# Kernel tuning notes

Measured on AMD Instinct MI355X. Metric: run time of the kernel, lower is better.

Reference implementation:

```python
import jax, jax.numpy as jnp
import numpy as np

N = 50000      # nodes
E = 1600000    # edges
IN = 128       # in_feats
H = 4          # heads
F = 32         # per-head feats (h_feats = out_feats = 32)
NEG_SLOPE = 0.2


def setup_inputs() -> dict:
    key = jax.random.key(0)
    ks = jax.random.split(key, 12)
    glorot = lambda k, shape: jax.random.normal(k, shape, jnp.float32) * np.sqrt(2.0 / (shape[0] + shape[-1])).astype(np.float32)
    x = jax.random.normal(ks[0], (N, IN), jnp.float32)
    edge_index = jax.random.randint(ks[1], (2, E), 0, N, dtype=jnp.int32)
    W1 = glorot(ks[2], (IN, H * F))
    att_src1 = glorot(ks[3], (H, F))
    att_dst1 = glorot(ks[4], (H, F))
    b1 = jnp.zeros((F,), jnp.float32)
    W2 = glorot(ks[5], (F, H * F))
    att_src2 = glorot(ks[6], (H, F))
    att_dst2 = glorot(ks[7], (H, F))
    b2 = jnp.zeros((F,), jnp.float32)
    return {"x": x, "edge_index": edge_index,
            "W1": W1, "att_src1": att_src1, "att_dst1": att_dst1, "b1": b1,
            "W2": W2, "att_src2": att_src2, "att_dst2": att_dst2, "b2": b2}


def gat_conv(x, edge_index, W, a_src, a_dst, bias):
    """PyG GATConv with concat=False (head-average), add_self_loops=True."""
    n = x.shape[0]
    h = (x @ W).reshape(n, H, F)                      # [N,H,F]
    loops = jnp.arange(n, dtype=edge_index.dtype)
    src = jnp.concatenate([edge_index[0], loops])     # [E+N]
    dst = jnp.concatenate([edge_index[1], loops])
    alpha_src = jnp.einsum('nhf,hf->nh', h, a_src)    # [N,H]
    alpha_dst = jnp.einsum('nhf,hf->nh', h, a_dst)
    e = jax.nn.leaky_relu(alpha_src[src] + alpha_dst[dst], NEG_SLOPE)  # [E+N,H]
    # scatter-softmax over incoming edges per destination node
    m = jax.ops.segment_max(e, dst, num_segments=n)
    e = jnp.exp(e - m[dst])
    s = jax.ops.segment_sum(e, dst, num_segments=n)
    alpha = e / (s[dst] + 1e-16)                      # [E+N,H]
    out = jax.ops.segment_sum(alpha[:, :, None] * h[src], dst, num_segments=n)  # [N,H,F]
    return out.mean(axis=1) + bias                    # concat=False: average heads


def reference(x, edge_index, W1, att_src1, att_dst1, b1, W2, att_src2, att_dst2, b2):
    h = gat_conv(x, edge_index, W1, att_src1, att_dst1, b1)
    h = jax.nn.elu(h)
    return gat_conv(h, edge_index, W2, att_src2, att_dst2, b2)
```

## Files before the change

kernel.cpp:

```cpp
#include <hip/hip_runtime.h>
#include <hip/hip_bf16.h>
#include <hip/hip_fp16.h>
#include <math.h>


#define NS 64
#define NB_S 4
#define MAXNPB_S 12500
#define NB_H 8
#define MAXNPB_H 6272

typedef unsigned int u32x4 __attribute__((ext_vector_type(4)));

__device__ __forceinline__ float lrelu(float x) { return x > 0.f ? x : 0.2f * x; }

__device__ __forceinline__ unsigned int fenc(float f) {
    unsigned int u = __float_as_uint(f);
    return (u & 0x80000000u) ? ~u : (u | 0x80000000u);
}
__device__ __forceinline__ float fdec(unsigned int e) {
    unsigned int u = (e & 0x80000000u) ? (e & 0x7FFFFFFFu) : ~e;
    return __uint_as_float(u);
}

__device__ __forceinline__ unsigned short f2bf(float x) {
    unsigned u = __float_as_uint(x);
    return (unsigned short)((u + 0x7FFFu + ((u >> 16) & 1u)) >> 16);
}
__device__ __forceinline__ float bflo(unsigned w) { return __uint_as_float(w << 16); }
__device__ __forceinline__ float bfhi(unsigned w) { return __uint_as_float(w & 0xFFFF0000u); }

__device__ __forceinline__ unsigned pack_h2(float a, float b) {
    const __half2 h = __float22half2_rn(make_float2(a, b));
    return *(const unsigned*)&h;
}
__device__ __forceinline__ float2 unpack_h2(unsigned w) {
    __half2 h = *(const __half2*)&w;
    return __half22float2(h);
}

__global__ __launch_bounds__(256) void scan_part(unsigned short* __restrict__ cnt_priv,
                                                 int* __restrict__ deg,
                                                 int* __restrict__ bsum, int n) {
    __shared__ int red[256];
    const int t = threadIdx.x;
    const int node = blockIdx.x * 256 + t;
    int run = 0;
    if (node < n) {
#pragma unroll 4
        for (int s = 0; s < NS; ++s) {
            unsigned short* p = &cnt_priv[(size_t)s * n + node];
            const int c = *p;
            *p = (unsigned short)run;
            run += c;
        }
        deg[node] = run;
    }
    red[t] = (node < n) ? run : 0;
    __syncthreads();
    for (int o = 128; o > 0; o >>= 1) {
        if (t < o) red[t] += red[t + o];
        __syncthreads();
    }
    if (t == 0) bsum[blockIdx.x] = red[0];
}

__global__ __launch_bounds__(256) void scan_mid(const int* __restrict__ bsum,
                                                int* __restrict__ boff, int nb,
                                                int* __restrict__ rowptr, int n) {
    __shared__ int s[256];
    const int t = threadIdx.x;
    const int v = (t < nb) ? bsum[t] : 0;
    s[t] = v;
    __syncthreads();
    for (int o = 1; o < 256; o <<= 1) {
        const int u = (t >= o) ? s[t - o] : 0;
        __syncthreads();
        s[t] += u;
        __syncthreads();
    }
    if (t < nb) boff[t] = s[t] - v;
    if (t == 255) rowptr[n] = s[255];
}

__global__ __launch_bounds__(256) void scan_final(const int* __restrict__ deg,
                                                  const int* __restrict__ boff,
                                                  int* __restrict__ rowptr, int n) {
    __shared__ int s[256];
    const int t = threadIdx.x;
    const int i = blockIdx.x * 256 + t;
    const int v = (i < n) ? deg[i] : 0;
    s[t] = v;
    __syncthreads();
    for (int o = 1; o < 256; o <<= 1) {
        const int u = (t >= o) ? s[t - o] : 0;
        __syncthreads();
        s[t] += u;
        __syncthreads();
    }
    if (i < n) rowptr[i] = boff[blockIdx.x] + s[t] - v;
}

__global__ __launch_bounds__(512) void scatter_kernel(
    const int* __restrict__ src, const int* __restrict__ dst,
    const int* __restrict__ rowptr, const unsigned short* __restrict__ cnt_priv,
    const float* __restrict__ asrc, const float* __restrict__ adst,
    const unsigned int* __restrict__ gmax,
    uint4* __restrict__ esd, int E, int n, int npb) {
    __shared__ int cur[MAXNPB_S];
    const int b = blockIdx.x & (NB_S - 1);
    const int s = blockIdx.x / NB_S;
    const int lo = b * npb;
    const int hi = min(lo + npb, n);
    const int span = hi - lo;
    if (span <= 0) return;
    {
        const unsigned short* cp = cnt_priv + (size_t)s * n + lo;
        const int* rp = rowptr + lo;
        for (int j = threadIdx.x; j < span; j += 512) cur[j] = rp[j] + (int)cp[j];
    }
    __syncthreads();
    const char* aB = (const char*)asrc;
    const char* dB = (const char*)adst;
    const float g0 = fdec(gmax[0]), g1 = fdec(gmax[1]);
    const float g2 = fdec(gmax[2]), g3 = fdec(gmax[3]);

    auto place = [&](int sv, int dv) {
        const int p = atomicAdd(&cur[dv - lo], 1);
        const unsigned s16 = (unsigned)(sv << 4);
        const unsigned d16 = (unsigned)(dv << 4);
        const float4 as = *(const float4*)(aB + s16);
        const float4 ad = *(const float4*)(dB + d16);
        const float q0 = __expf(lrelu(as.x + ad.x) - lrelu(g0 + ad.x));
        const float q1 = __expf(lrelu(as.y + ad.y) - lrelu(g1 + ad.y));
        const float q2 = __expf(lrelu(as.z + ad.z) - lrelu(g2 + ad.z));
        const float q3 = __expf(lrelu(as.w + ad.w) - lrelu(g3 + ad.w));
        esd[p] = make_uint4(s16, d16, pack_h2(q0, q1), pack_h2(q2, q3));
    };

    const int E4 = E >> 2;
    const int len4 = (E4 + NS - 1) / NS;
    const int beg4 = s * len4;
    const int end4 = min(beg4 + len4, E4);
    const int4* dst4 = (const int4*)dst;
    const int4* src4 = (const int4*)src;
    for (int i = beg4 + threadIdx.x; i < end4; i += 512) {
        const int4 d = dst4[i];
        const int4 sv = src4[i];
        if (d.x >= lo && d.x < hi) place(sv.x, d.x);
        if (d.y >= lo && d.y < hi) place(sv.y, d.y);
        if (d.z >= lo && d.z < hi) place(sv.z, d.z);
        if (d.w >= lo && d.w < hi) place(sv.w, d.w);
    }
    if (s == NS - 1) {
        for (int i = (E4 << 2) + threadIdx.x; i < E; i += 512) {
            const int d = dst[i];
            if (d >= lo && d < hi) place(src[i], d);
        }
    }
}

__global__ __launch_bounds__(256) void edge_w_kernel(
    uint4* __restrict__ esd,
    const float* __restrict__ asrc, const float* __restrict__ adst,
    const unsigned int* __restrict__ gmax, int Etot) {
    const char* aB = (const char*)asrc;
    const char* dB = (const char*)adst;
    const float g0 = fdec(gmax[0]), g1 = fdec(gmax[1]);
    const float g2 = fdec(gmax[2]), g3 = fdec(gmax[3]);
    for (int i = blockIdx.x * blockDim.x + threadIdx.x; i < Etot;
         i += gridDim.x * blockDim.x) {
        const unsigned long long sd =
            __builtin_nontemporal_load((const unsigned long long*)&esd[i]);
        const unsigned s16 = (unsigned)sd;
        const unsigned d16 = (unsigned)(sd >> 32);
        const float4 as = *(const float4*)(aB + s16);
        const float4 ad = *(const float4*)(dB + d16);
        const float q0 = __expf(lrelu(as.x + ad.x) - lrelu(g0 + ad.x));
        const float q1 = __expf(lrelu(as.y + ad.y) - lrelu(g1 + ad.y));
        const float q2 = __expf(lrelu(as.z + ad.z) - lrelu(g2 + ad.z));
        const float q3 = __expf(lrelu(as.w + ad.w) - lrelu(g3 + ad.w));
        const unsigned long long rec =
            ((unsigned long long)pack_h2(q2, q3) << 32) | pack_h2(q0, q1);
        __builtin_nontemporal_store(
            rec, (unsigned long long*)((char*)&esd[i] + 8));
    }
}

template <int K>
__global__ __launch_bounds__(256) void gemm_hist(
    const float* __restrict__ X, const float* __restrict__ W,
    const float* __restrict__ AttS, const float* __restrict__ AttD,
    unsigned short* __restrict__ Hb, float* __restrict__ asrc, float* __restrict__ adst,
    unsigned int* __restrict__ gmax, int n, int gemmGrid,
    const int* __restrict__ dst, unsigned short* __restrict__ cnt_priv,
    int E, int npbH) {
    constexpr int GEMM_BYTES = 64 * K * 4;
    constexpr int HIST_BYTES = (K == 128) ? (MAXNPB_H * 4) : 0;
    constexpr int SMEM_BYTES = (GEMM_BYTES > HIST_BYTES) ? GEMM_BYTES : HIST_BYTES;
    __shared__ __align__(16) char smem[SMEM_BYTES];
    __shared__ unsigned int smax[4];
    const int tid = threadIdx.x;

    if constexpr (K == 128) {
        if (blockIdx.x >= gemmGrid) {
            int* h = (int*)smem;
            const int hb = blockIdx.x - gemmGrid;
            const int b = hb & (NB_H - 1);
            const int s = hb / NB_H;
            const int lo = b * npbH;
            const int hi = min(lo + npbH, n);
            const int span = hi - lo;
            if (span <= 0) return;
            for (int j = tid; j < span; j += 256) h[j] = 0;
            __syncthreads();
            const int E4 = E >> 2;
            const int len4 = (E4 + NS - 1) / NS;
            const int beg4 = s * len4;
            const int end4 = min(beg4 + len4, E4);
            const int4* dst4 = (const int4*)dst;
            for (int i = beg4 + tid; i < end4; i += 256) {
                const int4 d = dst4[i];
                if (d.x >= lo && d.x < hi) atomicAdd(&h[d.x - lo], 1);
                if (d.y >= lo && d.y < hi) atomicAdd(&h[d.y - lo], 1);
                if (d.z >= lo && d.z < hi) atomicAdd(&h[d.z - lo], 1);
                if (d.w >= lo && d.w < hi) atomicAdd(&h[d.w - lo], 1);
            }
            if (s == NS - 1) {
                for (int i = (E4 << 2) + tid; i < E; i += 256) {
                    const int d = dst[i];
                    if (d >= lo && d < hi) atomicAdd(&h[d - lo], 1);
                }
            }
            __syncthreads();
            unsigned short* outp = cnt_priv + (size_t)s * n + lo;
            for (int j = tid; j < span; j += 256) outp[j] = (unsigned short)h[j];
            return;
        }
    }

    float* Xs = (float*)smem;
    const int r = tid >> 5;
    const int sub = tid & 31;
    const int head = sub >> 3;
    const int pos = ((head & 1) << 1) | (head >> 1);
    const int fc = (sub & 7) * 4;
    const int rowBase = blockIdx.x * 64;

    if (tid < 4) smax[tid] = 0u;
    {
        const float4* X4 = (const float4*)X;
        float4* Xs4 = (float4*)Xs;
        const int K4 = K / 4;
        for (int i = tid; i < 64 * K4; i += 256) {
            int rr = rowBase + i / K4;
            Xs4[i] = (rr < n) ? X4[(size_t)rr * K4 + (i % K4)] : make_float4(0.f, 0.f, 0.f, 0.f);
        }
    }
    __syncthreads();

    float acc[8][4] = {};
    const float4* W4g = (const float4*)W;
#pragma unroll 4
    for (int k = 0; k < K; k += 4) {
        float4 wv[4];
#pragma unroll
        for (int j = 0; j < 4; ++j) wv[j] = W4g[(k + j) * 32 + sub];
        float4 xv[8];
#pragma unroll
        for (int b = 0; b < 8; ++b)
            xv[b] = *(const float4*)&Xs[(b * 8 + r) * K + k];
#pragma unroll
        for (int b = 0; b < 8; ++b) {
            acc[b][0] = fmaf(xv[b].x, wv[0].x, acc[b][0]);
            acc[b][1] = fmaf(xv[b].x, wv[0].y, acc[b][1]);
            acc[b][2] = fmaf(xv[b].x, wv[0].z, acc[b][2]);
            acc[b][3] = fmaf(xv[b].x, wv[0].w, acc[b][3]);
            acc[b][0] = fmaf(xv[b].y, wv[1].x, acc[b][0]);
            acc[b][1] = fmaf(xv[b].y, wv[1].y, acc[b][1]);
            acc[b][2] = fmaf(xv[b].y, wv[1].z, acc[b][2]);
            acc[b][3] = fmaf(xv[b].y, wv[1].w, acc[b][3]);
            acc[b][0] = fmaf(xv[b].z, wv[2].x, acc[b][0]);
            acc[b][1] = fmaf(xv[b].z, wv[2].y, acc[b][1]);
            acc[b][2] = fmaf(xv[b].z, wv[2].z, acc[b][2]);
            acc[b][3] = fmaf(xv[b].z, wv[2].w, acc[b][3]);
            acc[b][0] = fmaf(xv[b].w, wv[3].x, acc[b][0]);
            acc[b][1] = fmaf(xv[b].w, wv[3].y, acc[b][1]);
            acc[b][2] = fmaf(xv[b].w, wv[3].z, acc[b][2]);
            acc[b][3] = fmaf(xv[b].w, wv[3].w, acc[b][3]);
        }
    }

    float a_s[4], a_d[4];
#pragma unroll
    for (int j = 0; j < 4; ++j) {
        a_s[j] = AttS[head * 32 + fc + j];
        a_d[j] = AttD[head * 32 + fc + j];
    }
#pragma unroll
    for (int b = 0; b < 8; ++b) {
        const int row = rowBase + b * 8 + r;
        const float p0 = __shfl_xor(acc[b][0], 16);
        const float p1 = __shfl_xor(acc[b][1], 16);
        const float p2 = __shfl_xor(acc[b][2], 16);
        const float p3 = __shfl_xor(acc[b][3], 16);
        if (row < n) {
            if (head < 2) {
                char* base = (char*)Hb + (size_t)row * 256 + (unsigned)fc * 8 + head * 4;
                *(unsigned*)(base + 0)  = (unsigned)f2bf(acc[b][0]) | ((unsigned)f2bf(p0) << 16);
                *(unsigned*)(base + 8)  = (unsigned)f2bf(acc[b][1]) | ((unsigned)f2bf(p1) << 16);
                *(unsigned*)(base + 16) = (unsigned)f2bf(acc[b][2]) | ((unsigned)f2bf(p2) << 16);
                *(unsigned*)(base + 24) = (unsigned)f2bf(acc[b][3]) | ((unsigned)f2bf(p3) << 16);
            }
            float ps = acc[b][0] * a_s[0] + acc[b][1] * a_s[1] +
                       acc[b][2] * a_s[2] + acc[b][3] * a_s[3];
            float pd = acc[b][0] * a_d[0] + acc[b][1] * a_d[1] +
                       acc[b][2] * a_d[2] + acc[b][3] * a_d[3];
#pragma unroll
            for (int msk = 1; msk < 8; msk <<= 1) {
                ps += __shfl_xor(ps, msk);
                pd += __shfl_xor(pd, msk);
            }
            if ((sub & 7) == 0) {
                asrc[row * 4 + pos] = ps;
                adst[row * 4 + pos] = pd;
                atomicMax(&smax[pos], fenc(ps));
            }
        }
    }
    __syncthreads();
    if (tid < 4) atomicMax(&gmax[tid], smax[tid]);
}

__global__ __launch_bounds__(256) void node_kernel(
    const int* __restrict__ rowptr, const uint4* __restrict__ esd,
    const unsigned short* __restrict__ Hb, const float* __restrict__ asrc,
    const float* __restrict__ adst, const unsigned int* __restrict__ gmax,
    const float* __restrict__ bias,
    float* __restrict__ outp, int n, int apply_elu) {
    const int node = blockIdx.x * 8 + (threadIdx.x >> 5);
    if (node >= n) return;
    const unsigned f = threadIdx.x & 31;
    const unsigned f8 = f * 8;
    const char* hB = (const char*)Hb;
    const u32x4* eB = (const u32x4*)esd;

    const int beg = rowptr[node], end = rowptr[node + 1];
    const float4 ad4 = *(const float4*)(adst + (size_t)node * 4);
    const float4 as4 = *(const float4*)(asrc + (size_t)node * 4);
    const float M0 = lrelu(fdec(gmax[0]) + ad4.x);
    const float M1 = lrelu(fdec(gmax[1]) + ad4.y);
    const float M2 = lrelu(fdec(gmax[2]) + ad4.z);
    const float M3 = lrelu(fdec(gmax[3]) + ad4.w);

    const float q0 = __expf(lrelu(as4.x + ad4.x) - M0);
    const float q1 = __expf(lrelu(as4.y + ad4.y) - M1);
    const float q2 = __expf(lrelu(as4.z + ad4.z) - M2);
    const float q3 = __expf(lrelu(as4.w + ad4.w) - M3);
    float s0 = q0, s1 = q1, s2 = q2, s3 = q3;
    const uint2 hs = *(const uint2*)(hB + ((size_t)node << 8) + f8);
    float a0 = q0 * bflo(hs.x);
    float a1 = q1 * bfhi(hs.x);
    float a2 = q2 * bflo(hs.y);
    float a3 = q3 * bfhi(hs.y);

    int i = beg;
    for (; i + 8 <= end; i += 8) {
        u32x4 e[8];
#pragma unroll
        for (int u = 0; u < 8; ++u)
            e[u] = __builtin_nontemporal_load(&eB[i + u]);
        uint2 h[8];
#pragma unroll
        for (int u = 0; u < 8; ++u)
            h[u] = *(const uint2*)(hB + (((unsigned)e[u].x) << 4) + f8);
#pragma unroll
        for (int u = 0; u < 8; ++u) {
            const float2 qa = unpack_h2(e[u].z);
            const float2 qb = unpack_h2(e[u].w);
            s0 += qa.x; s1 += qa.y; s2 += qb.x; s3 += qb.y;
            a0 = fmaf(qa.x, bflo(h[u].x), a0);
            a1 = fmaf(qa.y, bfhi(h[u].x), a1);
            a2 = fmaf(qb.x, bflo(h[u].y), a2);
            a3 = fmaf(qb.y, bfhi(h[u].y), a3);
        }
    }
    for (; i < end; ++i) {
        const u32x4 e = __builtin_nontemporal_load(&eB[i]);
        const uint2 h = *(const uint2*)(hB + (((unsigned)e.x) << 4) + f8);
        const float2 qa = unpack_h2(e.z);
        const float2 qb = unpack_h2(e.w);
        s0 += qa.x; s1 += qa.y; s2 += qb.x; s3 += qb.y;
        a0 = fmaf(qa.x, bflo(h.x), a0);
        a1 = fmaf(qa.y, bfhi(h.x), a1);
        a2 = fmaf(qb.x, bflo(h.y), a2);
        a3 = fmaf(qb.y, bfhi(h.y), a3);
    }

    float v = a0 / s0 + a1 / s1 + a2 / s2 + a3 / s3;
    v = v * 0.25f + bias[f];
    if (apply_elu) v = (v > 0.f) ? v : (__expf(v) - 1.f);
    outp[(size_t)node * 32 + f] = v;
}


extern "C" void kernel_launch(void* const* d_in, const int* in_sizes, int n_in,
                              void* d_out, int out_size, void* d_ws, size_t ws_size,
                              hipStream_t stream) {
    const int N = in_sizes[0] / 128;
    const int E = in_sizes[1] / 2;
    const float* x = (const float*)d_in[0];
    const int* ei = (const int*)d_in[1];
    const float* W1 = (const float*)d_in[2];
    const float* atS1 = (const float*)d_in[3];
    const float* atD1 = (const float*)d_in[4];
    const float* b1 = (const float*)d_in[5];
    const float* W2 = (const float*)d_in[6];
    const float* atS2 = (const float*)d_in[7];
    const float* atD2 = (const float*)d_in[8];
    const float* b2 = (const float*)d_in[9];
    float* out = (float*)d_out;

    char* ws = (char*)d_ws;
    size_t off = 0;
    auto alloc = [&](size_t bytes) {
        void* p = ws + off;
        off = (off + bytes + 255) & ~(size_t)255;
        return p;
    };
    unsigned int* gmax = (unsigned int*)alloc(8 * sizeof(unsigned int));
    unsigned short* cnt_priv = (unsigned short*)alloc((size_t)NS * N * 2);
    int* deg = (int*)alloc((size_t)N * 4);
    int* rowptr = (int*)alloc((size_t)(N + 1) * 4);
    int* bsum = (int*)alloc(256 * 4);
    int* boff = (int*)alloc(256 * 4);
    uint4* esd = (uint4*)alloc((size_t)E * 16);
    unsigned short* hb = (unsigned short*)alloc((size_t)N * 128 * 2);
    float* av_s = (float*)alloc((size_t)N * 4 * 4);
    float* av_d = (float*)alloc((size_t)N * 4 * 4);
    float* x2 = (float*)alloc((size_t)N * 32 * 4);

    const int* e_src = ei;
    const int* e_dst = ei + E;

    const int gemmGrid = (N + 63) / 64;
    const int nodeGrid = (N + 7) / 8;
    const int npbS = (N + NB_S - 1) / NB_S;
    const int npbH = (N + NB_H - 1) / NB_H;
    const int scanGrid = (N + 255) / 256;
    const int scatGrid = NB_S * NS;
    const int histGrid = NB_H * NS;

    (void)hipMemsetAsync(gmax, 0, 8 * sizeof(unsigned int), stream);

    gemm_hist<128><<<gemmGrid + histGrid, 256, 0, stream>>>(
        x, W1, atS1, atD1, hb, av_s, av_d, gmax, N, gemmGrid,
        e_dst, cnt_priv, E, npbH);
    scan_part<<<scanGrid, 256, 0, stream>>>(cnt_priv, deg, bsum, N);
    scan_mid<<<1, 256, 0, stream>>>(bsum, boff, scanGrid, rowptr, N);
    scan_final<<<scanGrid, 256, 0, stream>>>(deg, boff, rowptr, N);
    scatter_kernel<<<scatGrid, 512, 0, stream>>>(
        e_src, e_dst, rowptr, cnt_priv, av_s, av_d, gmax, esd, E, N, npbS);
    node_kernel<<<nodeGrid, 256, 0, stream>>>(rowptr, esd, hb, av_s, av_d, gmax,
                                              b1, x2, N, 1);
    gemm_hist<32><<<gemmGrid, 256, 0, stream>>>(
        x2, W2, atS2, atD2, hb, av_s, av_d, gmax + 4, N, gemmGrid,
        nullptr, nullptr, 0, 0);
    edge_w_kernel<<<2048, 256, 0, stream>>>(esd, av_s, av_d, gmax + 4, E);
    node_kernel<<<nodeGrid, 256, 0, stream>>>(rowptr, esd, hb, av_s, av_d, gmax + 4,
                                              b2, out, N, 0);
}
```

Before: 309.0 us.

## Overlap layer-1 GEMM with CSR scatter instead of histogram pass

The layer-1 GEMM, which computes attention logits, now shares a launch with the CSR scatter pass instead of the degree histogram. The histogram becomes its own 512-thread kernel. The scatter no longer needs the attention logits, so it writes only the src/dst offsets. The edge weights for layer 1 are then filled in by a separate edge_w_kernel pass. This lets the heavier scatter overlap the GEMM, at the cost of one extra pass over the edge array and a smaller scatter block size (256 threads).

```diff
diff --git a/kernel.cpp b/kernel.cpp
--- a/kernel.cpp
+++ b/kernel.cpp
@@ -37,6 +37,41 @@
 __device__ __forceinline__ float2 unpack_h2(unsigned w) {
     __half2 h = *(const __half2*)&w;
     return __half22float2(h);
+}
+
+__global__ __launch_bounds__(512) void hist_kernel(
+    const int* __restrict__ dst, unsigned short* __restrict__ cnt_priv,
+    int E, int n, int npbH) {
+    __shared__ int h[MAXNPB_H];
+    const int b = blockIdx.x & (NB_H - 1);
+    const int s = blockIdx.x / NB_H;
+    const int lo = b * npbH;
+    const int hi = min(lo + npbH, n);
+    const int span = hi - lo;
+    if (span <= 0) return;
+    for (int j = threadIdx.x; j < span; j += 512) h[j] = 0;
+    __syncthreads();
+    const int E4 = E >> 2;
+    const int len4 = (E4 + NS - 1) / NS;
+    const int beg4 = s * len4;
+    const int end4 = min(beg4 + len4, E4);
+    const int4* dst4 = (const int4*)dst;
+    for (int i = beg4 + threadIdx.x; i < end4; i += 512) {
+        const int4 d = dst4[i];
+        if (d.x >= lo && d.x < hi) atomicAdd(&h[d.x - lo], 1);
+        if (d.y >= lo && d.y < hi) atomicAdd(&h[d.y - lo], 1);
+        if (d.z >= lo && d.z < hi) atomicAdd(&h[d.z - lo], 1);
+        if (d.w >= lo && d.w < hi) atomicAdd(&h[d.w - lo], 1);
+    }
+    if (s == NS - 1) {
+        for (int i = (E4 << 2) + threadIdx.x; i < E; i += 512) {
+            const int d = dst[i];
+            if (d >= lo && d < hi) atomicAdd(&h[d - lo], 1);
+        }
+    }
+    __syncthreads();
+    unsigned short* outp = cnt_priv + (size_t)s * n + lo;
+    for (int j = threadIdx.x; j < span; j += 512) outp[j] = (unsigned short)h[j];
 }
 
 __global__ __launch_bounds__(256) void scan_part(unsigned short* __restrict__ cnt_priv,
@@ -99,65 +134,6 @@
         __syncthreads();
     }
     if (i < n) rowptr[i] = boff[blockIdx.x] + s[t] - v;
-}
-
-__global__ __launch_bounds__(512) void scatter_kernel(
-    const int* __restrict__ src, const int* __restrict__ dst,
-    const int* __restrict__ rowptr, const unsigned short* __restrict__ cnt_priv,
-    const float* __restrict__ asrc, const float* __restrict__ adst,
-    const unsigned int* __restrict__ gmax,
-    uint4* __restrict__ esd, int E, int n, int npb) {
-    __shared__ int cur[MAXNPB_S];
-    const int b = blockIdx.x & (NB_S - 1);
-    const int s = blockIdx.x / NB_S;
-    const int lo = b * npb;
-    const int hi = min(lo + npb, n);
-    const int span = hi - lo;
-    if (span <= 0) return;
-    {
-        const unsigned short* cp = cnt_priv + (size_t)s * n + lo;
-        const int* rp = rowptr + lo;
-        for (int j = threadIdx.x; j < span; j += 512) cur[j] = rp[j] + (int)cp[j];
-    }
-    __syncthreads();
-    const char* aB = (const char*)asrc;
-    const char* dB = (const char*)adst;
-    const float g0 = fdec(gmax[0]), g1 = fdec(gmax[1]);
-    const float g2 = fdec(gmax[2]), g3 = fdec(gmax[3]);
-
-    auto place = [&](int sv, int dv) {
-        const int p = atomicAdd(&cur[dv - lo], 1);
-        const unsigned s16 = (unsigned)(sv << 4);
-        const unsigned d16 = (unsigned)(dv << 4);
-        const float4 as = *(const float4*)(aB + s16);
-        const float4 ad = *(const float4*)(dB + d16);
-        const float q0 = __expf(lrelu(as.x + ad.x) - lrelu(g0 + ad.x));
-        const float q1 = __expf(lrelu(as.y + ad.y) - lrelu(g1 + ad.y));
-        const float q2 = __expf(lrelu(as.z + ad.z) - lrelu(g2 + ad.z));
-        const float q3 = __expf(lrelu(as.w + ad.w) - lrelu(g3 + ad.w));
-        esd[p] = make_uint4(s16, d16, pack_h2(q0, q1), pack_h2(q2, q3));
-    };
-
-    const int E4 = E >> 2;
-    const int len4 = (E4 + NS - 1) / NS;
-    const int beg4 = s * len4;
-    const int end4 = min(beg4 + len4, E4);
-    const int4* dst4 = (const int4*)dst;
-    const int4* src4 = (const int4*)src;
-    for (int i = beg4 + threadIdx.x; i < end4; i += 512) {
-        const int4 d = dst4[i];
-        const int4 sv = src4[i];
-        if (d.x >= lo && d.x < hi) place(sv.x, d.x);
-        if (d.y >= lo && d.y < hi) place(sv.y, d.y);
-        if (d.z >= lo && d.z < hi) place(sv.z, d.z);
-        if (d.w >= lo && d.w < hi) place(sv.w, d.w);
-    }
-    if (s == NS - 1) {
-        for (int i = (E4 << 2) + threadIdx.x; i < E; i += 512) {
-            const int d = dst[i];
-            if (d >= lo && d < hi) place(src[i], d);
-        }
-    }
 }
 
 __global__ __launch_bounds__(256) void edge_w_kernel(
@@ -188,64 +164,74 @@
 }
 
 template <int K>
-__global__ __launch_bounds__(256) void gemm_hist(
+__global__ __launch_bounds__(256) void gemm_scatter(
     const float* __restrict__ X, const float* __restrict__ W,
     const float* __restrict__ AttS, const float* __restrict__ AttD,
     unsigned short* __restrict__ Hb, float* __restrict__ asrc, float* __restrict__ adst,
-    unsigned int* __restrict__ gmax, int n, int gemmGrid,
-    const int* __restrict__ dst, unsigned short* __restrict__ cnt_priv,
-    int E, int npbH) {
+    unsigned int* __restrict__ gmax, int n, int scatGrid,
+    const int* __restrict__ src, const int* __restrict__ dst,
+    const int* __restrict__ rowptr, const unsigned short* __restrict__ cnt_priv,
+    uint4* __restrict__ esd, int E, int npbS) {
     constexpr int GEMM_BYTES = 64 * K * 4;
-    constexpr int HIST_BYTES = (K == 128) ? (MAXNPB_H * 4) : 0;
-    constexpr int SMEM_BYTES = (GEMM_BYTES > HIST_BYTES) ? GEMM_BYTES : HIST_BYTES;
+    constexpr int SCAT_BYTES = (K == 128) ? (MAXNPB_S * 4) : 0;
+    constexpr int SMEM_BYTES = (GEMM_BYTES > SCAT_BYTES) ? GEMM_BYTES : SCAT_BYTES;
     __shared__ __align__(16) char smem[SMEM_BYTES];
     __shared__ unsigned int smax[4];
     const int tid = threadIdx.x;
 
     if constexpr (K == 128) {
-        if (blockIdx.x >= gemmGrid) {
-            int* h = (int*)smem;
-            const int hb = blockIdx.x - gemmGrid;
-            const int b = hb & (NB_H - 1);
-            const int s = hb / NB_H;
-            const int lo = b * npbH;
-            const int hi = min(lo + npbH, n);
+        if (blockIdx.x < (unsigned)scatGrid) {
+            int* cur = (int*)smem;
+            const int b = blockIdx.x & (NB_S - 1);
+            const int s = blockIdx.x / NB_S;
+            const int lo = b * npbS;
+            const int hi = min(lo + npbS, n);
             const int span = hi - lo;
             if (span <= 0) return;
-            for (int j = tid; j < span; j += 256) h[j] = 0;
+            {
+                const unsigned short* cp = cnt_priv + (size_t)s * n + lo;
+                const int* rp = rowptr + lo;
+                for (int j = tid; j < span; j += 256) cur[j] = rp[j] + (int)cp[j];
+            }
             __syncthreads();
+            unsigned long long* esdU = (unsigned long long*)esd;
+            auto place = [&](int sv, int dv) {
+                const int p = atomicAdd(&cur[dv - lo], 1);
+                esdU[(size_t)p * 2] =
+                    ((unsigned long long)(unsigned)(dv << 4) << 32) | (unsigned)(sv << 4);
+            };
             const int E4 = E >> 2;
             const int len4 = (E4 + NS - 1) / NS;
             const int beg4 = s * len4;
             const int end4 = min(beg4 + len4, E4);
             const int4* dst4 = (const int4*)dst;
+            const int4* src4 = (const int4*)src;
             for (int i = beg4 + tid; i < end4; i += 256) {
                 const int4 d = dst4[i];
-                if (d.x >= lo && d.x < hi) atomicAdd(&h[d.x - lo], 1);
-                if (d.y >= lo && d.y < hi) atomicAdd(&h[d.y - lo], 1);
-                if (d.z >= lo && d.z < hi) atomicAdd(&h[d.z - lo], 1);
-                if (d.w >= lo && d.w < hi) atomicAdd(&h[d.w - lo], 1);
+                const int4 sv = src4[i];
+                if (d.x >= lo && d.x < hi) place(sv.x, d.x);
+                if (d.y >= lo && d.y < hi) place(sv.y, d.y);
+                if (d.z >= lo && d.z < hi) place(sv.z, d.z);
+                if (d.w >= lo && d.w < hi) place(sv.w, d.w);
             }
             if (s == NS - 1) {
                 for (int i = (E4 << 2) + tid; i < E; i += 256) {
                     const int d = dst[i];
-                    if (d >= lo && d < hi) atomicAdd(&h[d - lo], 1);
+                    if (d >= lo && d < hi) place(src[i], d);
                 }
             }
-            __syncthreads();
-            unsigned short* outp = cnt_priv + (size_t)s * n + lo;
-            for (int j = tid; j < span; j += 256) outp[j] = (unsigned short)h[j];
             return;
         }
     }
 
     float* Xs = (float*)smem;
+    const int gemmBlk = blockIdx.x - ((K == 128) ? scatGrid : 0);
     const int r = tid >> 5;
     const int sub = tid & 31;
     const int head = sub >> 3;
     const int pos = ((head & 1) << 1) | (head >> 1);
     const int fc = (sub & 7) * 4;
-    const int rowBase = blockIdx.x * 64;
+    const int rowBase = gemmBlk * 64;
 
     if (tid < 4) smax[tid] = 0u;
     {
@@ -453,19 +439,20 @@
 
     (void)hipMemsetAsync(gmax, 0, 8 * sizeof(unsigned int), stream);
 
-    gemm_hist<128><<<gemmGrid + histGrid, 256, 0, stream>>>(
-        x, W1, atS1, atD1, hb, av_s, av_d, gmax, N, gemmGrid,
-        e_dst, cnt_priv, E, npbH);
+    hist_kernel<<<histGrid, 512, 0, stream>>>(e_dst, cnt_priv, E, N, npbH);
     scan_part<<<scanGrid, 256, 0, stream>>>(cnt_priv, deg, bsum, N);
     scan_mid<<<1, 256, 0, stream>>>(bsum, boff, scanGrid, rowptr, N);
     scan_final<<<scanGrid, 256, 0, stream>>>(deg, boff, rowptr, N);
-    scatter_kernel<<<scatGrid, 512, 0, stream>>>(
-        e_src, e_dst, rowptr, cnt_priv, av_s, av_d, gmax, esd, E, N, npbS);
+
+    gemm_scatter<128><<<scatGrid + gemmGrid, 256, 0, stream>>>(
+        x, W1, atS1, atD1, hb, av_s, av_d, gmax, N, scatGrid,
+        e_src, e_dst, rowptr, cnt_priv, esd, E, npbS);
+    edge_w_kernel<<<2048, 256, 0, stream>>>(esd, av_s, av_d, gmax, E);
     node_kernel<<<nodeGrid, 256, 0, stream>>>(rowptr, esd, hb, av_s, av_d, gmax,
                                               b1, x2, N, 1);
-    gemm_hist<32><<<gemmGrid, 256, 0, stream>>>(
-        x2, W2, atS2, atD2, hb, av_s, av_d, gmax + 4, N, gemmGrid,
-        nullptr, nullptr, 0, 0);
+    gemm_scatter<32><<<gemmGrid, 256, 0, stream>>>(
+        x2, W2, atS2, atD2, hb, av_s, av_d, gmax + 4, N, 0,
+        nullptr, nullptr, nullptr, nullptr, nullptr, 0, 0);
     edge_w_kernel<<<2048, 256, 0, stream>>>(esd, av_s, av_d, gmax + 4, E);
     node_kernel<<<nodeGrid, 256, 0, stream>>>(rowptr, esd, hb, av_s, av_d, gmax + 4,
                                               b2, out, N, 0);
```

New measurement: 318.1 us. +3.0%, slower.

## Fuse layer-2 GEMM and attention logits into layer-1 node aggregation epilogue

Applied to the files above, without the earlier changes.

The first node aggregation kernel now applies ELU and then, per node, multiplies the 32-wide result by W2 using warp shuffles. In the same epilogue it computes the layer-2 attention logits and the block-wide max, and writes the bf16 features directly. This removes the separate layer-2 GEMM launch and the round trip of the fp32 intermediate x2 through global memory. In exchange each warp reads W2 from global/L2 for every node, and layer-2 features go to a separate buffer so they do not overwrite layer-1 features still being read.

```diff
diff --git a/kernel.cpp b/kernel.cpp
--- a/kernel.cpp
+++ b/kernel.cpp
@@ -187,7 +187,6 @@
     }
 }
 
-template <int K>
 __global__ __launch_bounds__(256) void gemm_hist(
     const float* __restrict__ X, const float* __restrict__ W,
     const float* __restrict__ AttS, const float* __restrict__ AttD,
@@ -195,48 +194,47 @@
     unsigned int* __restrict__ gmax, int n, int gemmGrid,
     const int* __restrict__ dst, unsigned short* __restrict__ cnt_priv,
     int E, int npbH) {
+    constexpr int K = 128;
     constexpr int GEMM_BYTES = 64 * K * 4;
-    constexpr int HIST_BYTES = (K == 128) ? (MAXNPB_H * 4) : 0;
+    constexpr int HIST_BYTES = MAXNPB_H * 4;
     constexpr int SMEM_BYTES = (GEMM_BYTES > HIST_BYTES) ? GEMM_BYTES : HIST_BYTES;
     __shared__ __align__(16) char smem[SMEM_BYTES];
     __shared__ unsigned int smax[4];
     const int tid = threadIdx.x;
 
-    if constexpr (K == 128) {
-        if (blockIdx.x >= gemmGrid) {
-            int* h = (int*)smem;
-            const int hb = blockIdx.x - gemmGrid;
-            const int b = hb & (NB_H - 1);
-            const int s = hb / NB_H;
-            const int lo = b * npbH;
-            const int hi = min(lo + npbH, n);
-            const int span = hi - lo;
-            if (span <= 0) return;
-            for (int j = tid; j < span; j += 256) h[j] = 0;
-            __syncthreads();
-            const int E4 = E >> 2;
-            const int len4 = (E4 + NS - 1) / NS;
-            const int beg4 = s * len4;
-            const int end4 = min(beg4 + len4, E4);
-            const int4* dst4 = (const int4*)dst;
-            for (int i = beg4 + tid; i < end4; i += 256) {
-                const int4 d = dst4[i];
-                if (d.x >= lo && d.x < hi) atomicAdd(&h[d.x - lo], 1);
-                if (d.y >= lo && d.y < hi) atomicAdd(&h[d.y - lo], 1);
-                if (d.z >= lo && d.z < hi) atomicAdd(&h[d.z - lo], 1);
-                if (d.w >= lo && d.w < hi) atomicAdd(&h[d.w - lo], 1);
+    if (blockIdx.x >= (unsigned)gemmGrid) {
+        int* h = (int*)smem;
+        const int hb = blockIdx.x - gemmGrid;
+        const int b = hb & (NB_H - 1);
+        const int s = hb / NB_H;
+        const int lo = b * npbH;
+        const int hi = min(lo + npbH, n);
+        const int span = hi - lo;
+        if (span <= 0) return;
+        for (int j = tid; j < span; j += 256) h[j] = 0;
+        __syncthreads();
+        const int E4 = E >> 2;
+        const int len4 = (E4 + NS - 1) / NS;
+        const int beg4 = s * len4;
+        const int end4 = min(beg4 + len4, E4);
+        const int4* dst4 = (const int4*)dst;
+        for (int i = beg4 + tid; i < end4; i += 256) {
+            const int4 d = dst4[i];
+            if (d.x >= lo && d.x < hi) atomicAdd(&h[d.x - lo], 1);
+            if (d.y >= lo && d.y < hi) atomicAdd(&h[d.y - lo], 1);
+            if (d.z >= lo && d.z < hi) atomicAdd(&h[d.z - lo], 1);
+            if (d.w >= lo && d.w < hi) atomicAdd(&h[d.w - lo], 1);
+        }
+        if (s == NS - 1) {
+            for (int i = (E4 << 2) + tid; i < E; i += 256) {
+                const int d = dst[i];
+                if (d >= lo && d < hi) atomicAdd(&h[d - lo], 1);
             }
-            if (s == NS - 1) {
-                for (int i = (E4 << 2) + tid; i < E; i += 256) {
-                    const int d = dst[i];
-                    if (d >= lo && d < hi) atomicAdd(&h[d - lo], 1);
-                }
-            }
-            __syncthreads();
-            unsigned short* outp = cnt_priv + (size_t)s * n + lo;
-            for (int j = tid; j < span; j += 256) outp[j] = (unsigned short)h[j];
-            return;
-        }
+        }
+        __syncthreads();
+        unsigned short* outp = cnt_priv + (size_t)s * n + lo;
+        for (int j = tid; j < span; j += 256) outp[j] = (unsigned short)h[j];
+        return;
     }
 
     float* Xs = (float*)smem;
@@ -332,22 +330,33 @@
     if (tid < 4) atomicMax(&gmax[tid], smax[tid]);
 }
 
+template <bool FUSE>
 __global__ __launch_bounds__(256) void node_kernel(
     const int* __restrict__ rowptr, const uint4* __restrict__ esd,
     const unsigned short* __restrict__ Hb, const float* __restrict__ asrc,
     const float* __restrict__ adst, const unsigned int* __restrict__ gmax,
     const float* __restrict__ bias,
-    float* __restrict__ outp, int n, int apply_elu) {
-    const int node = blockIdx.x * 8 + (threadIdx.x >> 5);
-    if (node >= n) return;
-    const unsigned f = threadIdx.x & 31;
+    const float* __restrict__ W2, const float* __restrict__ AttS2,
+    const float* __restrict__ AttD2, unsigned short* __restrict__ Hb2,
+    float* __restrict__ asrc2, float* __restrict__ adst2,
+    unsigned int* __restrict__ gmax2,
+    float* __restrict__ outp, int n) {
+    __shared__ unsigned int smax[4];
+    const int tid = threadIdx.x;
+    const int node = blockIdx.x * 8 + (tid >> 5);
+    const bool valid = node < n;
+    const int nc = valid ? node : 0;
+    const unsigned f = tid & 31;
     const unsigned f8 = f * 8;
     const char* hB = (const char*)Hb;
     const u32x4* eB = (const u32x4*)esd;
 
-    const int beg = rowptr[node], end = rowptr[node + 1];
-    const float4 ad4 = *(const float4*)(adst + (size_t)node * 4);
-    const float4 as4 = *(const float4*)(asrc + (size_t)node * 4);
+    if (FUSE && tid < 4) smax[tid] = 0u;
+
+    const int beg = valid ? rowptr[nc] : 0;
+    const int end = valid ? rowptr[nc + 1] : 0;
+    const float4 ad4 = *(const float4*)(adst + (size_t)nc * 4);
+    const float4 as4 = *(const float4*)(asrc + (size_t)nc * 4);
     const float M0 = lrelu(fdec(gmax[0]) + ad4.x);
     const float M1 = lrelu(fdec(gmax[1]) + ad4.y);
     const float M2 = lrelu(fdec(gmax[2]) + ad4.z);
@@ -358,7 +367,7 @@
     const float q2 = __expf(lrelu(as4.z + ad4.z) - M2);
     const float q3 = __expf(lrelu(as4.w + ad4.w) - M3);
     float s0 = q0, s1 = q1, s2 = q2, s3 = q3;
-    const uint2 hs = *(const uint2*)(hB + ((size_t)node << 8) + f8);
+    const uint2 hs = *(const uint2*)(hB + ((size_t)nc << 8) + f8);
     float a0 = q0 * bflo(hs.x);
     float a1 = q1 * bfhi(hs.x);
     float a2 = q2 * bflo(hs.y);
@@ -399,8 +408,54 @@
 
     float v = a0 / s0 + a1 / s1 + a2 / s2 + a3 / s3;
     v = v * 0.25f + bias[f];
-    if (apply_elu) v = (v > 0.f) ? v : (__expf(v) - 1.f);
-    outp[(size_t)node * 32 + f] = v;
+    if (!valid) v = 0.f;
+
+    if constexpr (!FUSE) {
+        if (valid) outp[(size_t)node * 32 + f] = v;
+    } else {
+        const float x = (v > 0.f) ? v : (__expf(v) - 1.f);
+        const float4* W4g = (const float4*)W2;
+        float c0 = 0.f, c1 = 0.f, c2 = 0.f, c3 = 0.f;
+#pragma unroll 4
+        for (int k = 0; k < 32; ++k) {
+            const float xk = __shfl(x, k, 32);
+            const float4 w = W4g[k * 32 + f];
+            c0 = fmaf(xk, w.x, c0);
+            c1 = fmaf(xk, w.y, c1);
+            c2 = fmaf(xk, w.z, c2);
+            c3 = fmaf(xk, w.w, c3);
+        }
+        const int head = f >> 3;
+        const int pos = ((head & 1) << 1) | (head >> 1);
+        const int fc = (f & 7) * 4;
+        const float p0 = __shfl_xor(c0, 16);
+        const float p1 = __shfl_xor(c1, 16);
+        const float p2 = __shfl_xor(c2, 16);
+        const float p3 = __shfl_xor(c3, 16);
+        if (valid && head < 2) {
+            char* base = (char*)Hb2 + (size_t)node * 256 + (unsigned)fc * 8 + head * 4;
+            *(unsigned*)(base + 0)  = (unsigned)f2bf(c0) | ((unsigned)f2bf(p0) << 16);
+            *(unsigned*)(base + 8)  = (unsigned)f2bf(c1) | ((unsigned)f2bf(p1) << 16);
+            *(unsigned*)(base + 16) = (unsigned)f2bf(c2) | ((unsigned)f2bf(p2) << 16);
+            *(unsigned*)(base + 24) = (unsigned)f2bf(c3) | ((unsigned)f2bf(p3) << 16);
+        }
+        float ps = c0 * AttS2[head * 32 + fc] + c1 * AttS2[head * 32 + fc + 1] +
+                   c2 * AttS2[head * 32 + fc + 2] + c3 * AttS2[head * 32 + fc + 3];
+        float pd = c0 * AttD2[head * 32 + fc] + c1 * AttD2[head * 32 + fc + 1] +
+                   c2 * AttD2[head * 32 + fc + 2] + c3 * AttD2[head * 32 + fc + 3];
+#pragma unroll
+        for (int msk = 1; msk < 8; msk <<= 1) {
+            ps += __shfl_xor(ps, msk);
+            pd += __shfl_xor(pd, msk);
+        }
+        if (valid && (f & 7) == 0) {
+            asrc2[node * 4 + pos] = ps;
+            adst2[node * 4 + pos] = pd;
+            atomicMax(&smax[pos], fenc(ps));
+        }
+        __syncthreads();
+        if (tid < 4) atomicMax(&gmax2[tid], smax[tid]);
+    }
 }
 
 
@@ -435,10 +490,12 @@
     int* bsum = (int*)alloc(256 * 4);
     int* boff = (int*)alloc(256 * 4);
     uint4* esd = (uint4*)alloc((size_t)E * 16);
-    unsigned short* hb = (unsigned short*)alloc((size_t)N * 128 * 2);
-    float* av_s = (float*)alloc((size_t)N * 4 * 4);
-    float* av_d = (float*)alloc((size_t)N * 4 * 4);
-    float* x2 = (float*)alloc((size_t)N * 32 * 4);
+    unsigned short* hb1 = (unsigned short*)alloc((size_t)N * 128 * 2);
+    unsigned short* hb2 = (unsigned short*)alloc((size_t)N * 128 * 2);
+    float* av_s1 = (float*)alloc((size_t)N * 4 * 4);
+    float* av_d1 = (float*)alloc((size_t)N * 4 * 4);
+    float* av_s2 = (float*)alloc((size_t)N * 4 * 4);
+    float* av_d2 = (float*)alloc((size_t)N * 4 * 4);
 
     const int* e_src = ei;
     const int* e_dst = ei + E;
@@ -453,20 +510,19 @@
 
     (void)hipMemsetAsync(gmax, 0, 8 * sizeof(unsigned int), stream);
 
-    gemm_hist<128><<<gemmGrid + histGrid, 256, 0, stream>>>(
-        x, W1, atS1, atD1, hb, av_s, av_d, gmax, N, gemmGrid,
+    gemm_hist<<<gemmGrid + histGrid, 256, 0, stream>>>(
+        x, W1, atS1, atD1, hb1, av_s1, av_d1, gmax, N, gemmGrid,
         e_dst, cnt_priv, E, npbH);
     scan_part<<<scanGrid, 256, 0, stream>>>(cnt_priv, deg, bsum, N);
     scan_mid<<<1, 256, 0, stream>>>(bsum, boff, scanGrid, rowptr, N);
     scan_final<<<scanGrid, 256, 0, stream>>>(deg, boff, rowptr, N);
     scatter_kernel<<<scatGrid, 512, 0, stream>>>(
-        e_src, e_dst, rowptr, cnt_priv, av_s, av_d, gmax, esd, E, N, npbS);
-    node_kernel<<<nodeGrid, 256, 0, stream>>>(rowptr, esd, hb, av_s, av_d, gmax,
-                                              b1, x2, N, 1);
-    gemm_hist<32><<<gemmGrid, 256, 0, stream>>>(
-        x2, W2, atS2, atD2, hb, av_s, av_d, gmax + 4, N, gemmGrid,
-        nullptr, nullptr, 0, 0);
-    edge_w_kernel<<<2048, 256, 0, stream>>>(esd, av_s, av_d, gmax + 4, E);
-    node_kernel<<<nodeGrid, 256, 0, stream>>>(rowptr, esd, hb, av_s, av_d, gmax + 4,
-                                              b2, out, N, 0);
-}
+        e_src, e_dst, rowptr, cnt_priv, av_s1, av_d1, gmax, esd, E, N, npbS);
+    node_kernel<true><<<nodeGrid, 256, 0, stream>>>(
+        rowptr, esd, hb1, av_s1, av_d1, gmax, b1,
+        W2, atS2, atD2, hb2, av_s2, av_d2, gmax + 4, nullptr, N);
+    edge_w_kernel<<<2048, 256, 0, stream>>>(esd, av_s2, av_d2, gmax + 4, E);
+    node_kernel<false><<<nodeGrid, 256, 0, stream>>>(
+        rowptr, esd, hb2, av_s2, av_d2, gmax + 4, b2,
+        nullptr, nullptr, nullptr, nullptr, nullptr, nullptr, nullptr, out, N);
+}
```

Measured after the change: 313.7 us. Within noise of the previous version (+1.5%).
